# Kernel tuning notes

Measured on AMD Instinct MI355X. Metric: run time of the kernel, lower is better.

Reference implementation:

```python
import jax, jax.numpy as jnp
import numpy as np

WS = 7        # window size (cubic)
SHIFT = 3     # shift size (cubic)
NH = 6        # num heads
EPS = 1e-5


def _layernorm(x, g, b):
    m = x.mean(-1, keepdims=True)
    v = ((x - m) ** 2).mean(-1, keepdims=True)
    return (x - m) / jnp.sqrt(v + EPS) * g + b


def _win_partition(x, ws):
    # (B,H,W,T,C) -> (B*nW, ws^3, C)
    B, H, W, T, C = x.shape
    x = x.reshape(B, H // ws, ws, W // ws, ws, T // ws, ws, C)
    return x.transpose(0, 1, 3, 5, 2, 4, 6, 7).reshape(-1, ws * ws * ws, C)


def _win_reverse(w, ws, B, H, W, T):
    # (B*nW, ws^3, C) -> (B,H,W,T,C)
    C = w.shape[-1]
    x = w.reshape(B, H // ws, W // ws, T // ws, ws, ws, ws, C)
    return x.transpose(0, 1, 4, 2, 5, 3, 6, 7).reshape(B, H, W, T, C)


def _rel_index(ws):
    # 3D relative position index, (N, N) int, N = ws^3 (torch.meshgrid default 'ij')
    coords = np.stack(np.meshgrid(np.arange(ws), np.arange(ws), np.arange(ws), indexing='ij'))
    cf = coords.reshape(3, -1)
    rel = (cf[:, :, None] - cf[:, None, :]).transpose(1, 2, 0)
    rel[:, :, 0] += ws - 1
    rel[:, :, 1] += ws - 1
    rel[:, :, 2] += ws - 1
    rel[:, :, 0] *= (2 * ws - 1) ** 2
    rel[:, :, 1] *= (2 * ws - 1)
    return rel.sum(-1)


def _compute_mask(Hp, Wp, Tp, ws, shift):
    img = np.zeros((1, Hp, Wp, Tp, 1), np.float32)
    cnt = 0
    sl = (slice(0, -ws), slice(-ws, -shift), slice(-shift, None))
    for h in sl:
        for w in sl:
            for t in sl:
                img[:, h, w, t, :] = cnt
                cnt += 1
    mw = np.asarray(_win_partition(jnp.asarray(img), ws)).reshape(-1, ws ** 3)  # (nW, N)
    am = mw[:, None, :] - mw[:, :, None]
    return jnp.asarray(np.where(am != 0, -100.0, 0.0).astype(np.float32))


def setup_inputs() -> dict:
    key = jax.random.key(0)
    ks = jax.random.split(key, 10)
    B, Hd, Wd, Td, C = 2, 28, 28, 28, 192
    L = Hd * Wd * Td
    Ch = int(C * 4.0)
    s = 0.02
    inp = {
        'x': jax.random.normal(ks[0], (B, L, C), jnp.float32),
        'mask': _compute_mask(Hd, Wd, Td, WS, SHIFT),
        'gamma1': jnp.ones((C,), jnp.float32),
        'beta1': jnp.zeros((C,), jnp.float32),
        'qkv_w': jax.random.normal(ks[1], (3 * C, C), jnp.float32) * s,
        'qkv_b': jnp.zeros((3 * C,), jnp.float32),
        'rpb_table': jax.random.normal(ks[2], ((2 * WS - 1) ** 3, NH), jnp.float32) * s,
        'proj_w': jax.random.normal(ks[3], (C, C), jnp.float32) * s,
        'proj_b': jnp.zeros((C,), jnp.float32),
        'gamma2': jnp.ones((C,), jnp.float32),
        'beta2': jnp.zeros((C,), jnp.float32),
        'fc1_w': jax.random.normal(ks[4], (Ch, C), jnp.float32) * s,
        'fc1_b': jnp.zeros((Ch,), jnp.float32),
        'fc2_w': jax.random.normal(ks[5], (C, Ch), jnp.float32) * s,
        'fc2_b': jnp.zeros((C,), jnp.float32),
        'H': Hd, 'W': Wd, 'T': Td,
    }
    return inp


def reference(x, mask, gamma1, beta1, qkv_w, qkv_b, rpb_table, proj_w, proj_b,
              gamma2, beta2, fc1_w, fc1_b, fc2_w, fc2_b, H, W, T):
    B, L, C = x.shape
    hd = C // NH
    scale = hd ** -0.5
    shortcut = x

    h1 = _layernorm(x, gamma1, beta1).reshape(B, H, W, T, C)
    # H,W,T are multiples of WS -> no padding; cyclic shift for SW-MSA
    shifted = jnp.roll(h1, (-SHIFT, -SHIFT, -SHIFT), axis=(1, 2, 3))
    xw = _win_partition(shifted, WS)            # (B*nW, N, C)
    Bn, N, _ = xw.shape

    qkv = (xw @ qkv_w.T + qkv_b).reshape(Bn, N, 3, NH, hd).transpose(2, 0, 3, 1, 4)
    q, k, v = qkv[0] * scale, qkv[1], qkv[2]     # (Bn, NH, N, hd)
    attn = jnp.einsum('bhnd,bhmd->bhnm', q, k)   # (Bn, NH, N, N)

    idx = _rel_index(WS)
    bias = rpb_table[idx.reshape(-1)].reshape(N, N, NH).transpose(2, 0, 1)
    attn = attn + bias[None]

    nW = mask.shape[0]
    attn = attn.reshape(Bn // nW, nW, NH, N, N) + mask[None, :, None]
    attn = jax.nn.softmax(attn.reshape(Bn, NH, N, N), axis=-1)

    out = jnp.einsum('bhnm,bhmd->bhnd', attn, v).transpose(0, 2, 1, 3).reshape(Bn, N, C)
    out = out @ proj_w.T + proj_b

    shifted = _win_reverse(out, WS, B, H, W, T)
    xr = jnp.roll(shifted, (SHIFT, SHIFT, SHIFT), axis=(1, 2, 3)).reshape(B, L, C)

    x = shortcut + xr
    h2 = _layernorm(x, gamma2, beta2)
    m = jax.nn.gelu(h2 @ fc1_w.T + fc1_b, approximate=False)
    return x + (m @ fc2_w.T + fc2_b)
```

## Files before the change

kernel.cpp:

```cpp
#include <hip/hip_runtime.h>
#include <hip/hip_bf16.h>

typedef unsigned short u16;
typedef unsigned int u32;
typedef __attribute__((ext_vector_type(8))) short s16x8;
typedef __attribute__((ext_vector_type(4))) float f32x4;

__device__ __forceinline__ float bf2f(u16 v) {
    union { u32 u; float f; } x; x.u = ((u32)v) << 16; return x.f;
}
__device__ __forceinline__ u16 f2bf(float f) {
    union { float f; u32 u; } x; x.f = f;
    u32 r = x.u + 0x7fffu + ((x.u >> 16) & 1u);
    return (u16)(r >> 16);
}
__device__ __forceinline__ u32 f2bf_pk(float a, float b) {
    __hip_bfloat162 hb = __float22bfloat162_rn(make_float2(a, b));
    union { __hip_bfloat162 h; u32 u; } c; c.h = hb; return c.u;
}
__device__ __forceinline__ void gl2lds(const u16* g, u16* l) {
    __builtin_amdgcn_global_load_lds(
        (const __attribute__((address_space(1))) unsigned int*)g,
        (__attribute__((address_space(3))) unsigned int*)l, 16, 0, 0);
}

#define L_TOK 21952
#define C_DIM 192
#define LOG2E 1.4426950408889634f
#define Q2SCALE 0.2550565444463649f

__global__ __launch_bounds__(256) void cvt_k(const float* __restrict__ s0,
                                             const float* __restrict__ s1,
                                             const float* __restrict__ s2,
                                             const float* __restrict__ s3,
                                             u16* __restrict__ dst)
{
    int i = blockIdx.x * 256 + threadIdx.x;
    float v;
    if (i < 110592) v = s0[i];
    else if (i < 147456) v = s1[i - 110592];
    else if (i < 294912) v = s2[i - 147456];
    else v = s3[i - 294912];
    dst[i] = f2bf(v);
}

__global__ __launch_bounds__(256) void bias6_k(const float* __restrict__ rpb,
                                               u16* __restrict__ bias6)
{
    const int m = blockIdx.x * 256 + threadIdx.x;
    if (m >= 343) return;
    const int n = blockIdx.y, hh = blockIdx.z;
    int hq = n / 49, r1 = n - hq * 49, wq = r1 / 7, tq = r1 - wq * 7;
    int hm = m / 49, r2 = m - hm * 49, wm = r2 / 7, tm = r2 - wm * 7;
    int idx = ((hq - hm + 6) * 13 + (wq - wm + 6)) * 13 + (tq - tm + 6);
    bias6[((size_t)hh * 343 + n) * 343 + m] = f2bf(rpb[idx * 6 + hh] * LOG2E);
}

template<int MODE>
__global__ __launch_bounds__(256) void ln_k(const float* __restrict__ in,
                                            const float* __restrict__ g,
                                            const float* __restrict__ b,
                                            u16* __restrict__ out)
{
    const int lane = threadIdx.x & 63, wv = threadIdx.x >> 6;
    const int tok = blockIdx.x * 4 + wv;
    size_t base = (size_t)tok * C_DIM;
    float x0 = in[base + lane];
    float x1 = in[base + 64 + lane];
    float x2 = in[base + 128 + lane];
    float s = x0 + x1 + x2;
    float sq = x0 * x0 + x1 * x1 + x2 * x2;
    #pragma unroll
    for (int off = 32; off > 0; off >>= 1) {
        s += __shfl_xor(s, off, 64);
        sq += __shfl_xor(sq, off, 64);
    }
    const float mean = s * (1.0f / 192.0f);
    float var = sq * (1.0f / 192.0f) - mean * mean;
    var = fmaxf(var, 0.0f);
    const float rstd = rsqrtf(var + 1e-5f);

    size_t obase;
    if (MODE == 0) {
        int bi = tok / L_TOK;
        int l = tok - bi * L_TOK;
        int h = l / 784;
        int rm = l - h * 784;
        int w = rm / 28;
        int t = rm - w * 28;
        int hs = h + 25; if (hs >= 28) hs -= 28;
        int ws = w + 25; if (ws >= 28) ws -= 28;
        int ts = t + 25; if (ts >= 28) ts -= 28;
        int win = ((bi * 4 + hs / 7) * 4 + ws / 7) * 4 + ts / 7;
        int n = (hs % 7) * 49 + (ws % 7) * 7 + (ts % 7);
        obase = ((size_t)win * 343 + n) * C_DIM;
    } else {
        obase = base;
    }
    #pragma unroll
    for (int i = 0; i < 3; i++) {
        int c = lane + i * 64;
        float xv = (i == 0) ? x0 : (i == 1) ? x1 : x2;
        float y = (xv - mean) * rstd * g[c] + b[c];
        out[obase + c] = f2bf(y);
    }
}

template<int K, int EPI>
__global__ __launch_bounds__(256) void gemm_k(const u16* __restrict__ A,
                                              const u16* __restrict__ W,
                                              const float* __restrict__ bias,
                                              void* __restrict__ outp,
                                              const void* __restrict__ resp,
                                              int Ncols)
{
    __shared__ __align__(16) u16 As[128 * 32];
    __shared__ __align__(16) u16 Bs[64 * 32];
    const int t = threadIdx.x;
    const int bm = blockIdx.y;
    const int n0 = blockIdx.x * 64;
    const int lane = t & 63, wv = t >> 6;
    const int wm = (wv >> 1) * 64, wn = (wv & 1) * 32;
    const int r16 = lane & 15, quad = lane >> 4;

    f32x4 acc[4][2];
    #pragma unroll
    for (int i = 0; i < 4; i++)
        #pragma unroll
        for (int j = 0; j < 2; j++) acc[i][j] = (f32x4){0.f, 0.f, 0.f, 0.f};

    const int ar = t >> 2, ac = (t & 3) * 8;
    const size_t abase = (size_t)bm * 128 * K;

    for (int k0 = 0; k0 < K; k0 += 32) {
        gl2lds(&A[abase + (size_t)ar * K + k0 + ac], &As[8 * t]);
        gl2lds(&A[abase + (size_t)(ar + 64) * K + k0 + ac], &As[2048 + 8 * t]);
        gl2lds(&W[(size_t)(n0 + ar) * K + k0 + ac], &Bs[8 * t]);
        __syncthreads();
        s16x8 af[4], bf[2];
        #pragma unroll
        for (int fm = 0; fm < 4; fm++)
            af[fm] = *(const s16x8*)&As[(wm + fm * 16 + r16) * 32 + quad * 8];
        #pragma unroll
        for (int fn = 0; fn < 2; fn++)
            bf[fn] = *(const s16x8*)&Bs[(wn + fn * 16 + r16) * 32 + quad * 8];
        #pragma unroll
        for (int fm = 0; fm < 4; fm++)
            #pragma unroll
            for (int fn = 0; fn < 2; fn++)
                acc[fm][fn] = __builtin_amdgcn_mfma_f32_16x16x32_bf16(af[fm], bf[fn], acc[fm][fn], 0, 0, 0);
        __syncthreads();
    }

    #pragma unroll
    for (int fm = 0; fm < 4; fm++) {
        #pragma unroll
        for (int fn = 0; fn < 2; fn++) {
            #pragma unroll
            for (int r = 0; r < 4; r++) {
                const int grow = bm * 128 + wm + fm * 16 + quad * 4 + r;
                const int gcol = n0 + wn + fn * 16 + r16;
                float v = acc[fm][fn][r] + bias[gcol];
                if (EPI == 0) {
                    if (gcol < 192) v *= Q2SCALE;
                    ((u16*)outp)[(size_t)grow * Ncols + gcol] = f2bf(v);
                } else if (EPI == 1) {
                    v = 0.5f * v * (1.0f + erff(v * 0.70710678118654752f));
                    ((u16*)outp)[(size_t)grow * Ncols + gcol] = f2bf(v);
                } else if (EPI == 2) {
                    size_t o = (size_t)grow * C_DIM + gcol;
                    ((float*)outp)[o] = v + ((const float*)resp)[o];
                } else {
                    int win = grow / 343, n = grow - win * 343;
                    int bi = win >> 6, wi = win & 63;
                    int hw = wi >> 4, ww = (wi >> 2) & 3, tw = wi & 3;
                    int ph = n / 49, rem = n - ph * 49;
                    int pw = rem / 7, pt = rem - pw * 7;
                    int h = hw * 7 + ph + 3; if (h >= 28) h -= 28;
                    int w = ww * 7 + pw + 3; if (w >= 28) w -= 28;
                    int tt = tw * 7 + pt + 3; if (tt >= 28) tt -= 28;
                    int l = (h * 28 + w) * 28 + tt;
                    size_t o = ((size_t)bi * L_TOK + l) * C_DIM + gcol;
                    ((float*)outp)[o] = v + ((const float*)resp)[o];
                }
            }
        }
    }
}

__global__ __launch_bounds__(256, 2) void attn_k(const u16* __restrict__ qkv,
                                                 const u16* __restrict__ bias6,
                                                 u16* __restrict__ out)
{
    __shared__ __align__(16) u16 Ks[352 * 40];
    __shared__ __align__(16) u16 Vt[32 * 360];
    __shared__ __align__(16) u16 Pb[4][16 * 40];
    __shared__ u16 Cn[344];

    const int hh = blockIdx.x;
    const int win = blockIdx.y;
    const int wi = win & 63;
    const int t = threadIdx.x, lane = t & 63, wv = t >> 6;
    const int r16 = lane & 15, quad = lane >> 4;
    const size_t qbase = (size_t)win * 343 * 576 + hh * 32;

    for (int j = t; j < 343 * 4; j += 256) {
        int m = j >> 2, ch = j & 3;
        *(uint4*)&Ks[m * 40 + ch * 8] = *(const uint4*)&qkv[qbase + (size_t)m * 576 + 192 + ch * 8];
    }
    if (t < 36) {
        int m = 343 + (t >> 2), ch = t & 3;
        *(uint4*)&Ks[m * 40 + ch * 8] = (uint4){0u, 0u, 0u, 0u};
    }
    for (int i = t; i < 343 * 16; i += 256) {
        int m = i >> 4, d2 = (i & 15) * 2;
        int pm = (m & ~31) + 2 * (m & 15) + ((m >> 4) & 1);
        u32 w2 = *(const u32*)&qkv[qbase + (size_t)m * 576 + 384 + d2];
        Vt[d2 * 360 + pm] = (u16)(w2 & 0xffffu);
        Vt[(d2 + 1) * 360 + pm] = (u16)(w2 >> 16);
    }
    for (int i = t; i < 32 * 9; i += 256) {
        int d = i / 9, m = 343 + i % 9;
        int pm = (m & ~31) + 2 * (m & 15) + ((m >> 4) & 1);
        Vt[d * 360 + pm] = 0;
    }
    {
        const int hw = (wi >> 4) & 3, ww = (wi >> 2) & 3, tw = wi & 3;
        for (int n = t; n < 344; n += 256) {
            int nn = n > 342 ? 342 : n;
            int ph = nn / 49, rem = nn - ph * 49;
            int pw = rem / 7, pt = rem - pw * 7;
            int rh = (hw == 3) ? (ph < 4 ? 1 : 2) : 0;
            int rw = (ww == 3) ? (pw < 4 ? 1 : 2) : 0;
            int rt = (tw == 3) ? (pt < 4 ? 1 : 2) : 0;
            Cn[n] = (u16)(rh * 9 + rw * 3 + rt);
        }
    }
    __syncthreads();

    const u16* biash = bias6 + (size_t)hh * 343 * 343;

    u16 cntc[22];
    #pragma unroll
    for (int fn = 0; fn < 22; fn++) {
        int col = fn * 16 + r16; if (col > 342) col = 342;
        cntc[fn] = Cn[col];
    }

    for (int qt = 0; qt < 6; qt++) {
        const int row0 = qt * 64 + wv * 16;
        int qrow = row0 + r16; if (qrow > 342) qrow = 342;
        s16x8 qa = *(const s16x8*)&qkv[qbase + (size_t)qrow * 576 + quad * 8];

        u16 cr[4];
        #pragma unroll
        for (int r = 0; r < 4; r++) {
            int n = row0 + quad * 4 + r; if (n > 342) n = 342;
            cr[r] = Cn[n];
        }

        f32x4 sacc[22];
        #pragma unroll
        for (int fn = 0; fn < 22; fn++) {
            int col = fn * 16 + r16; if (col > 342) col = 342;
            #pragma unroll
            for (int r = 0; r < 4; r++) {
                int n = row0 + quad * 4 + r; if (n > 342) n = 342;
                sacc[fn][r] = bf2f(biash[(size_t)n * 343 + col]);
            }
        }
        #pragma unroll
        for (int fn = 0; fn < 22; fn++) {
            s16x8 kb = *(const s16x8*)&Ks[(fn * 16 + r16) * 40 + quad * 8];
            sacc[fn] = __builtin_amdgcn_mfma_f32_16x16x32_bf16(qa, kb, sacc[fn], 0, 0, 0);
        }

        float rowsum[4] = {0.f, 0.f, 0.f, 0.f};
        #pragma unroll
        for (int fn = 0; fn < 22; fn++) {
            const int col = fn * 16 + r16;
            #pragma unroll
            for (int r = 0; r < 4; r++) {
                float p = 0.0f;
                if (col < 343 && cntc[fn] == cr[r])
                    p = exp2f(fminf(sacc[fn][r], 42.0f));
                sacc[fn][r] = p;
                rowsum[r] += p;
            }
        }
        #pragma unroll
        for (int r = 0; r < 4; r++) {
            float v = rowsum[r];
            #pragma unroll
            for (int off = 1; off < 16; off <<= 1) v += __shfl_xor(v, off, 64);
            rowsum[r] = v;
        }

        u16* pw = &Pb[wv][0];
        u32* pw32 = (u32*)pw;
        f32x4 oacc0 = (f32x4){0.f, 0.f, 0.f, 0.f};
        f32x4 oacc1 = (f32x4){0.f, 0.f, 0.f, 0.f};
        #pragma unroll
        for (int c = 0; c < 11; c++) {
            asm volatile("s_waitcnt lgkmcnt(0)" ::: "memory");
            #pragma unroll
            for (int r = 0; r < 4; r++)
                pw32[(quad * 4 + r) * 20 + r16] = f2bf_pk(sacc[2 * c][r], sacc[2 * c + 1][r]);
            asm volatile("s_waitcnt lgkmcnt(0)" ::: "memory");
            s16x8 pa = *(const s16x8*)&pw[r16 * 40 + quad * 8];
            s16x8 vb0 = *(const s16x8*)&Vt[r16 * 360 + c * 32 + quad * 8];
            s16x8 vb1 = *(const s16x8*)&Vt[(16 + r16) * 360 + c * 32 + quad * 8];
            oacc0 = __builtin_amdgcn_mfma_f32_16x16x32_bf16(pa, vb0, oacc0, 0, 0, 0);
            oacc1 = __builtin_amdgcn_mfma_f32_16x16x32_bf16(pa, vb1, oacc1, 0, 0, 0);
        }

        #pragma unroll
        for (int r = 0; r < 4; r++) {
            const int n = row0 + quad * 4 + r;
            if (n < 343) {
                const float rs = rowsum[r];
                const float inv = rs > 0.0f ? 1.0f / rs : 0.0f;
                size_t o = ((size_t)win * 343 + n) * C_DIM + hh * 32;
                out[o + r16] = f2bf(oacc0[r] * inv);
                out[o + 16 + r16] = f2bf(oacc1[r] * inv);
            }
        }
    }
}

extern "C" void kernel_launch(void* const* d_in, const int* in_sizes, int n_in,
                              void* d_out, int out_size, void* d_ws, size_t ws_size,
                              hipStream_t stream)
{
    const float* x      = (const float*)d_in[0];
    const float* g1     = (const float*)d_in[2];
    const float* b1     = (const float*)d_in[3];
    const float* qkv_w  = (const float*)d_in[4];
    const float* qkv_b  = (const float*)d_in[5];
    const float* rpb    = (const float*)d_in[6];
    const float* proj_w = (const float*)d_in[7];
    const float* proj_b = (const float*)d_in[8];
    const float* g2     = (const float*)d_in[9];
    const float* b2     = (const float*)d_in[10];
    const float* fc1_w  = (const float*)d_in[11];
    const float* fc1_b  = (const float*)d_in[12];
    const float* fc2_w  = (const float*)d_in[13];
    const float* fc2_b  = (const float*)d_in[14];

    char* ws = (char*)d_ws;
    u16* xw        = (u16*)(ws + 0);
    u16* bias6     = (u16*)(ws + 0);
    u16* qkv       = (u16*)(ws + 16861184);
    u16* a1        = (u16*)(ws + 0);
    u16* attn_out  = (u16*)(ws + 67444736);
    u16* h2        = attn_out;
    float* x2      = (float*)(ws + 84305920);
    u16* wbf       = (u16*)(ws + 118028288);
    u16* qkv_wb = wbf;
    u16* proj_wb = wbf + 110592;
    u16* fc1_wb = wbf + 147456;
    u16* fc2_wb = wbf + 294912;

    cvt_k<<<dim3(1728), 256, 0, stream>>>(qkv_w, proj_w, fc1_w, fc2_w, wbf);
    ln_k<0><<<dim3(10976), 256, 0, stream>>>(x, g1, b1, xw);
    gemm_k<192, 0><<<dim3(9, 343), 256, 0, stream>>>(xw, qkv_wb, qkv_b, qkv, nullptr, 576);
    bias6_k<<<dim3(2, 343, 6), 256, 0, stream>>>(rpb, bias6);
    attn_k<<<dim3(6, 128), 256, 0, stream>>>(qkv, bias6, attn_out);
    gemm_k<192, 3><<<dim3(3, 343), 256, 0, stream>>>(attn_out, proj_wb, proj_b, x2, x, 192);
    ln_k<1><<<dim3(10976), 256, 0, stream>>>(x2, g2, b2, h2);
    gemm_k<192, 1><<<dim3(12, 343), 256, 0, stream>>>(h2, fc1_wb, fc1_b, a1, nullptr, 768);
    gemm_k<768, 2><<<dim3(3, 343), 256, 0, stream>>>(a1, fc2_wb, fc2_b, d_out, x2, 192);
}
```

Baseline: 369.5 us.

## Transpose bias table for vector loads, batch GEMM k-steps, skip empty tiles

The relative-position bias table is now stored transposed and padded, so each lane fetches its four row values with one 8-byte load instead of four scattered 2-byte loads. The GEMM stages three 32-wide k-slices into LDS per barrier pair, which cuts synchronisations and triples shared-memory use per block. The attention kernel skips query tiles that lie wholly past the 343 valid rows. The packed bf16 conversion now uses a manual rounding helper. Larger LDS may lower GEMM occupancy.

```diff
diff --git a/kernel.cpp b/kernel.cpp
--- a/kernel.cpp
+++ b/kernel.cpp
@@ -15,8 +15,7 @@
     return (u16)(r >> 16);
 }
 __device__ __forceinline__ u32 f2bf_pk(float a, float b) {
-    __hip_bfloat162 hb = __float22bfloat162_rn(make_float2(a, b));
-    union { __hip_bfloat162 h; u32 u; } c; c.h = hb; return c.u;
+    return (u32)f2bf(a) | ((u32)f2bf(b) << 16);
 }
 __device__ __forceinline__ void gl2lds(const u16* g, u16* l) {
     __builtin_amdgcn_global_load_lds(
@@ -28,6 +27,7 @@
 #define C_DIM 192
 #define LOG2E 1.4426950408889634f
 #define Q2SCALE 0.2550565444463649f
+#define BT_STR 352
 
 __global__ __launch_bounds__(256) void cvt_k(const float* __restrict__ s0,
                                              const float* __restrict__ s1,
@@ -45,15 +45,19 @@
 }
 
 __global__ __launch_bounds__(256) void bias6_k(const float* __restrict__ rpb,
-                                               u16* __restrict__ bias6)
-{
-    const int m = blockIdx.x * 256 + threadIdx.x;
-    if (m >= 343) return;
-    const int n = blockIdx.y, hh = blockIdx.z;
-    int hq = n / 49, r1 = n - hq * 49, wq = r1 / 7, tq = r1 - wq * 7;
-    int hm = m / 49, r2 = m - hm * 49, wm = r2 / 7, tm = r2 - wm * 7;
-    int idx = ((hq - hm + 6) * 13 + (wq - wm + 6)) * 13 + (tq - tm + 6);
-    bias6[((size_t)hh * 343 + n) * 343 + m] = f2bf(rpb[idx * 6 + hh] * LOG2E);
+                                               u16* __restrict__ bias6T)
+{
+    const int n = blockIdx.x * 256 + threadIdx.x;
+    if (n >= BT_STR) return;
+    const int m = blockIdx.y, hh = blockIdx.z;
+    u16 v = 0;
+    if (n <= 342) {
+        int hq = n / 49, r1 = n - hq * 49, wq = r1 / 7, tq = r1 - wq * 7;
+        int hm = m / 49, r2 = m - hm * 49, wm = r2 / 7, tm = r2 - wm * 7;
+        int idx = ((hq - hm + 6) * 13 + (wq - wm + 6)) * 13 + (tq - tm + 6);
+        v = f2bf(rpb[idx * 6 + hh] * LOG2E);
+    }
+    bias6T[((size_t)hh * 343 + m) * BT_STR + n] = v;
 }
 
 template<int MODE>
@@ -114,8 +118,8 @@
                                               const void* __restrict__ resp,
                                               int Ncols)
 {
-    __shared__ __align__(16) u16 As[128 * 32];
-    __shared__ __align__(16) u16 Bs[64 * 32];
+    __shared__ __align__(16) u16 As[3 * 128 * 32];
+    __shared__ __align__(16) u16 Bs[3 * 64 * 32];
     const int t = threadIdx.x;
     const int bm = blockIdx.y;
     const int n0 = blockIdx.x * 64;
@@ -132,24 +136,31 @@
     const int ar = t >> 2, ac = (t & 3) * 8;
     const size_t abase = (size_t)bm * 128 * K;
 
-    for (int k0 = 0; k0 < K; k0 += 32) {
-        gl2lds(&A[abase + (size_t)ar * K + k0 + ac], &As[8 * t]);
-        gl2lds(&A[abase + (size_t)(ar + 64) * K + k0 + ac], &As[2048 + 8 * t]);
-        gl2lds(&W[(size_t)(n0 + ar) * K + k0 + ac], &Bs[8 * t]);
+    for (int kc = 0; kc < K; kc += 96) {
+        if (kc) __syncthreads();
+        #pragma unroll
+        for (int kt = 0; kt < 3; kt++) {
+            const int k0 = kc + kt * 32;
+            gl2lds(&A[abase + (size_t)ar * K + k0 + ac], &As[kt * 4096 + 8 * t]);
+            gl2lds(&A[abase + (size_t)(ar + 64) * K + k0 + ac], &As[kt * 4096 + 2048 + 8 * t]);
+            gl2lds(&W[(size_t)(n0 + ar) * K + k0 + ac], &Bs[kt * 2048 + 8 * t]);
+        }
         __syncthreads();
-        s16x8 af[4], bf[2];
-        #pragma unroll
-        for (int fm = 0; fm < 4; fm++)
-            af[fm] = *(const s16x8*)&As[(wm + fm * 16 + r16) * 32 + quad * 8];
-        #pragma unroll
-        for (int fn = 0; fn < 2; fn++)
-            bf[fn] = *(const s16x8*)&Bs[(wn + fn * 16 + r16) * 32 + quad * 8];
-        #pragma unroll
-        for (int fm = 0; fm < 4; fm++)
+        #pragma unroll
+        for (int kt = 0; kt < 3; kt++) {
+            s16x8 af[4], bf[2];
+            #pragma unroll
+            for (int fm = 0; fm < 4; fm++)
+                af[fm] = *(const s16x8*)&As[kt * 4096 + (wm + fm * 16 + r16) * 32 + quad * 8];
             #pragma unroll
             for (int fn = 0; fn < 2; fn++)
-                acc[fm][fn] = __builtin_amdgcn_mfma_f32_16x16x32_bf16(af[fm], bf[fn], acc[fm][fn], 0, 0, 0);
-        __syncthreads();
+                bf[fn] = *(const s16x8*)&Bs[kt * 2048 + (wn + fn * 16 + r16) * 32 + quad * 8];
+            #pragma unroll
+            for (int fm = 0; fm < 4; fm++)
+                #pragma unroll
+                for (int fn = 0; fn < 2; fn++)
+                    acc[fm][fn] = __builtin_amdgcn_mfma_f32_16x16x32_bf16(af[fm], bf[fn], acc[fm][fn], 0, 0, 0);
+        }
     }
 
     #pragma unroll
@@ -189,7 +200,7 @@
 }
 
 __global__ __launch_bounds__(256, 2) void attn_k(const u16* __restrict__ qkv,
-                                                 const u16* __restrict__ bias6,
+                                                 const u16* __restrict__ bias6T,
                                                  u16* __restrict__ out)
 {
     __shared__ __align__(16) u16 Ks[352 * 40];
@@ -238,7 +249,7 @@
     }
     __syncthreads();
 
-    const u16* biash = bias6 + (size_t)hh * 343 * 343;
+    const u16* biashT = bias6T + (size_t)hh * 343 * BT_STR;
 
     u16 cntc[22];
     #pragma unroll
@@ -249,13 +260,15 @@
 
     for (int qt = 0; qt < 6; qt++) {
         const int row0 = qt * 64 + wv * 16;
+        if (row0 > 342) continue;
         int qrow = row0 + r16; if (qrow > 342) qrow = 342;
         s16x8 qa = *(const s16x8*)&qkv[qbase + (size_t)qrow * 576 + quad * 8];
 
+        const int n0 = row0 + quad * 4;
         u16 cr[4];
         #pragma unroll
         for (int r = 0; r < 4; r++) {
-            int n = row0 + quad * 4 + r; if (n > 342) n = 342;
+            int n = n0 + r; if (n > 342) n = 342;
             cr[r] = Cn[n];
         }
 
@@ -263,11 +276,11 @@
         #pragma unroll
         for (int fn = 0; fn < 22; fn++) {
             int col = fn * 16 + r16; if (col > 342) col = 342;
-            #pragma unroll
-            for (int r = 0; r < 4; r++) {
-                int n = row0 + quad * 4 + r; if (n > 342) n = 342;
-                sacc[fn][r] = bf2f(biash[(size_t)n * 343 + col]);
-            }
+            uint2 bv = *(const uint2*)&biashT[(size_t)col * BT_STR + n0];
+            sacc[fn][0] = bf2f((u16)(bv.x & 0xffffu));
+            sacc[fn][1] = bf2f((u16)(bv.x >> 16));
+            sacc[fn][2] = bf2f((u16)(bv.y & 0xffffu));
+            sacc[fn][3] = bf2f((u16)(bv.y >> 16));
         }
         #pragma unroll
         for (int fn = 0; fn < 22; fn++) {
@@ -316,7 +329,7 @@
 
         #pragma unroll
         for (int r = 0; r < 4; r++) {
-            const int n = row0 + quad * 4 + r;
+            const int n = n0 + r;
             if (n < 343) {
                 const float rs = rowsum[r];
                 const float inv = rs > 0.0f ? 1.0f / rs : 0.0f;
@@ -349,7 +362,7 @@
 
     char* ws = (char*)d_ws;
     u16* xw        = (u16*)(ws + 0);
-    u16* bias6     = (u16*)(ws + 0);
+    u16* bias6T    = (u16*)(ws + 0);
     u16* qkv       = (u16*)(ws + 16861184);
     u16* a1        = (u16*)(ws + 0);
     u16* attn_out  = (u16*)(ws + 67444736);
@@ -364,8 +377,8 @@
     cvt_k<<<dim3(1728), 256, 0, stream>>>(qkv_w, proj_w, fc1_w, fc2_w, wbf);
     ln_k<0><<<dim3(10976), 256, 0, stream>>>(x, g1, b1, xw);
     gemm_k<192, 0><<<dim3(9, 343), 256, 0, stream>>>(xw, qkv_wb, qkv_b, qkv, nullptr, 576);
-    bias6_k<<<dim3(2, 343, 6), 256, 0, stream>>>(rpb, bias6);
-    attn_k<<<dim3(6, 128), 256, 0, stream>>>(qkv, bias6, attn_out);
+    bias6_k<<<dim3(2, 343, 6), 256, 0, stream>>>(rpb, bias6T);
+    attn_k<<<dim3(6, 128), 256, 0, stream>>>(qkv, bias6T, attn_out);
     gemm_k<192, 3><<<dim3(3, 343), 256, 0, stream>>>(attn_out, proj_wb, proj_b, x2, x, 192);
     ln_k<1><<<dim3(10976), 256, 0, stream>>>(x2, g2, b2, h2);
     gemm_k<192, 1><<<dim3(12, 343), 256, 0, stream>>>(h2, fc1_wb, fc1_b, a1, nullptr, 768);
```

New measurement: 367.1 us. About the same (-0.6%).
